# Kernel tuning notes

Hardware: AMD Instinct MI355X
Metric: run time of the kernel (lower is better)

The kernel has to match this reference:

```python
import jax, jax.numpy as jnp
import numpy as np

B, D, W, H = 512, 128, 256, 256  # batch, drive_num, window_size, hidden_size


def setup_inputs() -> dict:
    key = jax.random.key(0)
    k = jax.random.split(key, 7)
    x = jax.random.normal(k[0], (B, D, W), jnp.float32)
    # encode_attn: Linear(window_size + 2*hidden_size, 1)
    attn_w = jax.random.normal(k[1], (W + 2 * H,), jnp.float32) * 0.02
    attn_b = jax.random.normal(k[2], (), jnp.float32) * 0.02
    # single-layer LSTM, input_size=D, hidden_size=H; PyTorch gate order i,f,g,o
    W_ih = jax.random.normal(k[3], (4 * H, D), jnp.float32) * 0.05
    W_hh = jax.random.normal(k[4], (4 * H, H), jnp.float32) * 0.05
    b_ih = jax.random.normal(k[5], (4 * H,), jnp.float32) * 0.05
    b_hh = jax.random.normal(k[6], (4 * H,), jnp.float32) * 0.05
    return {"x": x, "attn_w": attn_w, "attn_b": attn_b,
            "W_ih": W_ih, "W_hh": W_hh, "b_ih": b_ih, "b_hh": b_hh}


def reference(x, attn_w, attn_b, W_ih, W_hh, b_ih, b_hh):
    # x: [B, D, W]
    h_dim = W_hh.shape[1]
    w_h = attn_w[:h_dim]           # weight on repeated hidden state
    w_c = attn_w[h_dim:2 * h_dim]  # weight on repeated cell state
    w_x = attn_w[2 * h_dim:]       # weight on full input row (constant over t)
    # precompute input contribution to attention logits: [B, D]
    e_x = jnp.einsum('bdw,w->bd', x, w_x) + attn_b
    x_steps = jnp.moveaxis(x, 2, 0)  # [W, B, D]

    def step(carry, x_t):
        h, c = carry  # [B, H] each
        # attention logit: h/c terms broadcast over drive dim
        e = e_x + (h @ w_h + c @ w_c)[:, None]  # [B, D]
        a = jax.nn.softmax(e, axis=-1)
        x_hat = a * x_t  # [B, D]
        gates = x_hat @ W_ih.T + b_ih + h @ W_hh.T + b_hh  # [B, 4H]
        i, f, g, o = jnp.split(gates, 4, axis=-1)
        c_new = jax.nn.sigmoid(f) * c + jax.nn.sigmoid(i) * jnp.tanh(g)
        h_new = jax.nn.sigmoid(o) * jnp.tanh(c_new)
        return (h_new, c_new), h_new

    bsz = x.shape[0]
    h0 = jnp.zeros((bsz, h_dim), x.dtype)
    c0 = jnp.zeros((bsz, h_dim), x.dtype)
    _, hs = jax.lax.scan(step, (h0, c0), x_steps)  # hs: [W, B, H]
    return jnp.transpose(hs, (1, 0, 2))  # [B, W, H] == hidden_states[:, 1:]
```

## Files before the change

### kernel.cpp

```cpp
#include <hip/hip_runtime.h>
#include <cstdint>

#define NB 512
#define ND 128
#define NW 256
#define NH 256
#define PGRP 32
#define QGRP 8

typedef _Float16 f16;
typedef _Float16 h8 __attribute__((ext_vector_type(8)));
typedef float f32x4 __attribute__((ext_vector_type(4)));

__device__ __forceinline__ float sigm(float v){ return 1.f/(1.f+__expf(-v)); }
__device__ __forceinline__ float tanh_fast(float v){
  v = fminf(fmaxf(v,-15.f),15.f);
  float e = __expf(2.f*v);
  return (e-1.f)/(e+1.f);
}

__global__ __launch_bounds__(128) void attn_kernel(
    const float* __restrict__ x, const float* __restrict__ attn_w,
    const float* __restrict__ attn_b, float* __restrict__ a_buf)
{
    __shared__ float wx[NW];
    __shared__ float sred[2];
    const int b = blockIdx.x;
    const int d = threadIdx.x;

    wx[d]       = attn_w[2 * NH + d];
    wx[d + 128] = attn_w[2 * NH + d + 128];
    __syncthreads();

    const float4* xr = (const float4*)(x + ((size_t)b * ND + d) * NW);
    float acc = 0.f;
    #pragma unroll 8
    for (int w4 = 0; w4 < NW / 4; ++w4) {
        float4 v = xr[w4];
        acc += v.x * wx[w4*4+0] + v.y * wx[w4*4+1]
             + v.z * wx[w4*4+2] + v.w * wx[w4*4+3];
    }
    float e = acc + attn_b[0];

    float mx = e;
    #pragma unroll
    for (int o = 32; o > 0; o >>= 1) mx = fmaxf(mx, __shfl_xor(mx, o));
    if ((d & 63) == 0) sred[d >> 6] = mx;
    __syncthreads();
    mx = fmaxf(sred[0], sred[1]);
    __syncthreads();

    float p = __expf(e - mx);
    float s = p;
    #pragma unroll
    for (int o = 32; o > 0; o >>= 1) s += __shfl_xor(s, o);
    if ((d & 63) == 0) sred[d >> 6] = s;
    __syncthreads();
    s = sred[0] + sred[1];

    a_buf[(size_t)b * ND + d] = p / s;
}

__global__ __launch_bounds__(512) void pack_kernel(
    const float* __restrict__ W_ih, const float* __restrict__ W_hh,
    const float* __restrict__ b_ih, const float* __restrict__ b_hh,
    f16* __restrict__ Wfrag, float* __restrict__ bias)
{
    int flat = blockIdx.x * 512 + threadIdx.x;
    int l    = flat & 63;
    int kt   = (flat >> 6) % 12;
    int wq   = (flat >> 6) / 12;
    int col16 = l & 15, kb = l >> 4;
    int hcol = (wq >> 3) * 32 + (wq & 7) * 4 + (col16 >> 2);
    int gate = col16 & 3;
    int n    = gate * 256 + hcol;
    int k0   = kt * 32 + kb * 8;

    f16 tmp[8];
    #pragma unroll
    for (int e = 0; e < 8; ++e) {
        int k = k0 + e;
        float v = (k < NH) ? W_hh[(size_t)n * NH + k]
                           : W_ih[(size_t)n * ND + (k - NH)];
        tmp[e] = (f16)v;
    }
    *(h8*)(Wfrag + (size_t)flat * 8) = *(const h8*)tmp;

    if (flat < 1024) bias[flat] = b_ih[flat] + b_hh[flat];
}

__global__ __launch_bounds__(512) void init_kernel(unsigned* __restrict__ flags)
{
    flags[blockIdx.x * 512 + threadIdx.x] = 0u;
}

__global__ __launch_bounds__(512, 2) void lstm_kernel(
    const float* __restrict__ x, const float* __restrict__ a_buf,
    const float* __restrict__ bias, const f16* __restrict__ Wfrag,
    f16* __restrict__ hx, unsigned* __restrict__ flags,
    float* __restrict__ out)
{
    __shared__ __align__(16) unsigned char A16[16 * 768];
    __shared__ float scr[8][272];

    const int tid = threadIdx.x;
    const int w = tid >> 6, l = tid & 63;
    const int p = blockIdx.x & 31, q = blockIdx.x >> 5;

    h8 bfrag[12];
    {
        const h8* wsrc = (const h8*)Wfrag + ((q * 8 + w) * 12) * 64 + l;
        #pragma unroll
        for (int kt = 0; kt < 12; ++kt) bfrag[kt] = wsrc[kt * 64];
    }

    const int m = l >> 2, hh = l & 3;
    const int jcol = q * 32 + w * 4 + hh;
    float bias4[4];
    #pragma unroll
    for (int g = 0; g < 4; ++g) bias4[g] = bias[g * 256 + jcol];
    float cstate = 0.f;

    float areg[8];
    const float* xbase = nullptr;
    const int xrow = tid >> 4, xdc = tid & 15;
    if (tid < 256) {
        int b = p * 16 + xrow;
        #pragma unroll
        for (int e = 0; e < 8; ++e) areg[e] = a_buf[b * ND + xdc * 8 + e];
        xbase = x + ((size_t)b * ND + xdc * 8) * NW;
    }
    const int r2 = tid >> 5, kc = tid & 31;
    const int arow = l & 15, akb = l >> 4;

    float4 xq[8];

    for (int t = 0; t < NW; ++t) {
        if (tid < 256 && (t & 3) == 0) {
            #pragma unroll
            for (int e = 0; e < 8; ++e)
                xq[e] = *(const float4*)(xbase + (size_t)e * NW + t);
        }
        if (tid < 256) {
            f16 xv[8];
            #pragma unroll
            for (int e = 0; e < 8; ++e) {
                float xf = xq[e].x;
                xq[e] = make_float4(xq[e].y, xq[e].z, xq[e].w, xq[e].x);
                xv[e] = (f16)(xf * areg[e]);
            }
            int byte = xrow * 768 + 512 + xdc * 16;
            byte ^= (xrow & 7) << 4;
            *(h8*)(A16 + byte) = *(const h8*)xv;
        }
        {
            int byte = r2 * 768 + kc * 16;
            byte ^= (r2 & 7) << 4;
            if (t == 0) {
                ((unsigned long long*)(A16 + byte))[0] = 0ull;
                ((unsigned long long*)(A16 + byte))[1] = 0ull;
            } else {
                while (__hip_atomic_load(&flags[(t - 1) * PGRP + p],
                                         __ATOMIC_RELAXED, __HIP_MEMORY_SCOPE_AGENT) < 8u) {}
                const unsigned long long* hrow = (const unsigned long long*)
                    (hx + ((size_t)((t - 1) & 1) * NB + p * 16 + r2) * NH);
                unsigned long long d0 = __hip_atomic_load(hrow + kc * 2 + 0,
                        __ATOMIC_RELAXED, __HIP_MEMORY_SCOPE_AGENT);
                unsigned long long d1 = __hip_atomic_load(hrow + kc * 2 + 1,
                        __ATOMIC_RELAXED, __HIP_MEMORY_SCOPE_AGENT);
                ((unsigned long long*)(A16 + byte))[0] = d0;
                ((unsigned long long*)(A16 + byte))[1] = d1;
            }
        }
        __syncthreads();

        f32x4 acc = {0.f, 0.f, 0.f, 0.f};
        #pragma unroll
        for (int kt = 0; kt < 12; ++kt) {
            int byte = arow * 768 + kt * 64 + akb * 16;
            byte ^= (arow & 7) << 4;
            h8 afrag = *(const h8*)(A16 + byte);
            acc = __builtin_amdgcn_mfma_f32_16x16x32_f16(afrag, bfrag[kt], acc, 0, 0, 0);
        }

        {
            float* sw = &scr[w][0];
            int col = l & 15, rb = (l >> 4) * 4;
            sw[(rb + 0) * 17 + col] = acc[0];
            sw[(rb + 1) * 17 + col] = acc[1];
            sw[(rb + 2) * 17 + col] = acc[2];
            sw[(rb + 3) * 17 + col] = acc[3];
            asm volatile("s_waitcnt lgkmcnt(0)" ::: "memory");
            float G0 = sw[m * 17 + hh * 4 + 0] + bias4[0];
            float G1 = sw[m * 17 + hh * 4 + 1] + bias4[1];
            float G2 = sw[m * 17 + hh * 4 + 2] + bias4[2];
            float G3 = sw[m * 17 + hh * 4 + 3] + bias4[3];
            float ig = sigm(G0), fg = sigm(G1);
            float gg = tanh_fast(G2), og = sigm(G3);
            cstate = fg * cstate + ig * gg;
            float hn = og * tanh_fast(cstate);

            int brow = p * 16 + m;
            __builtin_nontemporal_store(hn, &out[((size_t)brow * NW + t) * NH + jcol]);

            f16 hf = (f16)hn;
            unsigned short hb = __builtin_bit_cast(unsigned short, hf);
            int other = __shfl_xor((int)hb, 1);
            if (!(l & 1)) {
                unsigned val = (unsigned)hb | ((unsigned)(unsigned short)other << 16);
                unsigned* dst = (unsigned*)((unsigned short*)hx
                                + ((size_t)(t & 1) * NB + brow) * NH + jcol);
                __hip_atomic_store(dst, val, __ATOMIC_RELAXED, __HIP_MEMORY_SCOPE_AGENT);
            }
        }
        __syncthreads();
        if (tid == 0 && t < NW - 1)
            atomicAdd(&flags[t * PGRP + p], 1u);
    }
}

extern "C" void kernel_launch(void* const* d_in, const int* in_sizes, int n_in,
                              void* d_out, int out_size, void* d_ws, size_t ws_size,
                              hipStream_t stream) {
    (void)in_sizes; (void)n_in; (void)out_size;

    const float* x      = (const float*)d_in[0];
    const float* attn_w = (const float*)d_in[1];
    const float* attn_b = (const float*)d_in[2];
    const float* W_ih   = (const float*)d_in[3];
    const float* W_hh   = (const float*)d_in[4];
    const float* b_ih   = (const float*)d_in[5];
    const float* b_hh   = (const float*)d_in[6];
    float* out = (float*)d_out;

    char* ws = (char*)d_ws;
    float*    a_buf = (float*)ws;
    float*    bias  = (float*)(ws + 262144);
    f16*      Wfrag = (f16*)(ws + 266240);
    f16*      hx    = (f16*)(ws + 1052672);
    unsigned* flags = (unsigned*)(ws + 1576960);
    if (ws_size < (size_t)1609728) return;

    attn_kernel<<<NB, 128, 0, stream>>>(x, attn_w, attn_b, a_buf);
    pack_kernel<<<96, 512, 0, stream>>>(W_ih, W_hh, b_ih, b_hh, Wfrag, bias);
    init_kernel<<<16, 512, 0, stream>>>(flags);
    lstm_kernel<<<PGRP * QGRP, 512, 0, stream>>>(x, a_buf, bias, Wfrag, hx, flags, out);
}
```

Baseline: 828.3 us.

## Overlap x-part MFMAs with h wait and use per-block byte flags

Restructures the recurrent step so the input-projection MFMAs (k tiles 8..11) run before the next hidden state arrives, and the x staging for step t+1 is done after the flag publish instead of on the critical path. Replaces the atomicAdd counter with a u64 flag where each of the 8 column blocks sets its own byte, polled by a single thread against a full mask. The output store is also moved after the flag publish. This aims to shorten the per-step cross-block dependency latency, at the cost of an explicit vmcnt wait and a larger flag buffer, and it relies on byte stores into the u64 being seen correctly by the polling load.

```diff
diff --git a/kernel.cpp b/kernel.cpp
--- a/kernel.cpp
+++ b/kernel.cpp
@@ -11,6 +11,9 @@
 typedef _Float16 f16;
 typedef _Float16 h8 __attribute__((ext_vector_type(8)));
 typedef float f32x4 __attribute__((ext_vector_type(4)));
+typedef unsigned long long u64;
+
+#define FLAG_DONE 0x0101010101010101ull
 
 __device__ __forceinline__ float sigm(float v){ return 1.f/(1.f+__expf(-v)); }
 __device__ __forceinline__ float tanh_fast(float v){
@@ -97,7 +100,7 @@
 __global__ __launch_bounds__(512, 2) void lstm_kernel(
     const float* __restrict__ x, const float* __restrict__ a_buf,
     const float* __restrict__ bias, const f16* __restrict__ Wfrag,
-    f16* __restrict__ hx, unsigned* __restrict__ flags,
+    f16* __restrict__ hx, u64* __restrict__ flags,
     float* __restrict__ out)
 {
     __shared__ __align__(16) unsigned char A16[16 * 768];
@@ -135,54 +138,75 @@
 
     float4 xq[8];
 
+    {
+        int byte = r2 * 768 + kc * 16;
+        byte ^= (r2 & 7) << 4;
+        h8 z = {};
+        *(h8*)(A16 + byte) = z;
+    }
+    if (tid < 256) {
+        #pragma unroll
+        for (int e = 0; e < 8; ++e)
+            xq[e] = *(const float4*)(xbase + (size_t)e * NW);
+        f16 xv[8];
+        #pragma unroll
+        for (int e = 0; e < 8; ++e) {
+            float xf = xq[e].x;
+            xq[e] = make_float4(xq[e].y, xq[e].z, xq[e].w, xq[e].x);
+            xv[e] = (f16)(xf * areg[e]);
+        }
+        int byte = xrow * 768 + 512 + xdc * 16;
+        byte ^= (xrow & 7) << 4;
+        *(h8*)(A16 + byte) = *(const h8*)xv;
+    }
+
     for (int t = 0; t < NW; ++t) {
-        if (tid < 256 && (t & 3) == 0) {
+        if (t > 0 && tid == 0) {
+            while (__hip_atomic_load(&flags[(t - 1) * PGRP + p],
+                                     __ATOMIC_RELAXED, __HIP_MEMORY_SCOPE_AGENT)
+                   != FLAG_DONE) {}
+        }
+        __syncthreads();
+
+        f32x4 acc = {0.f, 0.f, 0.f, 0.f};
+        if (t > 0) {
+            const u64* hrow = (const u64*)
+                (hx + ((size_t)((t - 1) & 1) * NB + p * 16 + r2) * NH);
+            u64 d0 = __hip_atomic_load(hrow + kc * 2 + 0,
+                    __ATOMIC_RELAXED, __HIP_MEMORY_SCOPE_AGENT);
+            u64 d1 = __hip_atomic_load(hrow + kc * 2 + 1,
+                    __ATOMIC_RELAXED, __HIP_MEMORY_SCOPE_AGENT);
             #pragma unroll
-            for (int e = 0; e < 8; ++e)
-                xq[e] = *(const float4*)(xbase + (size_t)e * NW + t);
-        }
-        if (tid < 256) {
-            f16 xv[8];
-            #pragma unroll
-            for (int e = 0; e < 8; ++e) {
-                float xf = xq[e].x;
-                xq[e] = make_float4(xq[e].y, xq[e].z, xq[e].w, xq[e].x);
-                xv[e] = (f16)(xf * areg[e]);
-            }
-            int byte = xrow * 768 + 512 + xdc * 16;
-            byte ^= (xrow & 7) << 4;
-            *(h8*)(A16 + byte) = *(const h8*)xv;
-        }
-        {
+            for (int kt = 8; kt < 12; ++kt) {
+                int byte = arow * 768 + kt * 64 + akb * 16;
+                byte ^= (arow & 7) << 4;
+                h8 afrag = *(const h8*)(A16 + byte);
+                acc = __builtin_amdgcn_mfma_f32_16x16x32_f16(afrag, bfrag[kt], acc, 0, 0, 0);
+            }
             int byte = r2 * 768 + kc * 16;
             byte ^= (r2 & 7) << 4;
-            if (t == 0) {
-                ((unsigned long long*)(A16 + byte))[0] = 0ull;
-                ((unsigned long long*)(A16 + byte))[1] = 0ull;
-            } else {
-                while (__hip_atomic_load(&flags[(t - 1) * PGRP + p],
-                                         __ATOMIC_RELAXED, __HIP_MEMORY_SCOPE_AGENT) < 8u) {}
-                const unsigned long long* hrow = (const unsigned long long*)
-                    (hx + ((size_t)((t - 1) & 1) * NB + p * 16 + r2) * NH);
-                unsigned long long d0 = __hip_atomic_load(hrow + kc * 2 + 0,
-                        __ATOMIC_RELAXED, __HIP_MEMORY_SCOPE_AGENT);
-                unsigned long long d1 = __hip_atomic_load(hrow + kc * 2 + 1,
-                        __ATOMIC_RELAXED, __HIP_MEMORY_SCOPE_AGENT);
-                ((unsigned long long*)(A16 + byte))[0] = d0;
-                ((unsigned long long*)(A16 + byte))[1] = d1;
+            ((u64*)(A16 + byte))[0] = d0;
+            ((u64*)(A16 + byte))[1] = d1;
+        } else {
+            #pragma unroll
+            for (int kt = 8; kt < 12; ++kt) {
+                int byte = arow * 768 + kt * 64 + akb * 16;
+                byte ^= (arow & 7) << 4;
+                h8 afrag = *(const h8*)(A16 + byte);
+                acc = __builtin_amdgcn_mfma_f32_16x16x32_f16(afrag, bfrag[kt], acc, 0, 0, 0);
             }
         }
         __syncthreads();
 
-        f32x4 acc = {0.f, 0.f, 0.f, 0.f};
-        #pragma unroll
-        for (int kt = 0; kt < 12; ++kt) {
+        #pragma unroll
+        for (int kt = 0; kt < 8; ++kt) {
             int byte = arow * 768 + kt * 64 + akb * 16;
             byte ^= (arow & 7) << 4;
             h8 afrag = *(const h8*)(A16 + byte);
             acc = __builtin_amdgcn_mfma_f32_16x16x32_f16(afrag, bfrag[kt], acc, 0, 0, 0);
         }
 
+        float hn;
         {
             float* sw = &scr[w][0];
             int col = l & 15, rb = (l >> 4) * 4;
@@ -198,10 +222,7 @@
             float ig = sigm(G0), fg = sigm(G1);
             float gg = tanh_fast(G2), og = sigm(G3);
             cstate = fg * cstate + ig * gg;
-            float hn = og * tanh_fast(cstate);
-
-            int brow = p * 16 + m;
-            __builtin_nontemporal_store(hn, &out[((size_t)brow * NW + t) * NH + jcol]);
+            hn = og * tanh_fast(cstate);
 
             f16 hf = (f16)hn;
             unsigned short hb = __builtin_bit_cast(unsigned short, hf);
@@ -209,13 +230,38 @@
             if (!(l & 1)) {
                 unsigned val = (unsigned)hb | ((unsigned)(unsigned short)other << 16);
                 unsigned* dst = (unsigned*)((unsigned short*)hx
-                                + ((size_t)(t & 1) * NB + brow) * NH + jcol);
+                                + ((size_t)(t & 1) * NB + p * 16 + m) * NH + jcol);
                 __hip_atomic_store(dst, val, __ATOMIC_RELAXED, __HIP_MEMORY_SCOPE_AGENT);
             }
         }
+        asm volatile("s_waitcnt vmcnt(0)" ::: "memory");
         __syncthreads();
-        if (tid == 0 && t < NW - 1)
-            atomicAdd(&flags[t * PGRP + p], 1u);
+
+        if (tid == 0) {
+            unsigned char* fb = ((unsigned char*)&flags[t * PGRP + p]) + q;
+            __hip_atomic_store(fb, (unsigned char)1,
+                               __ATOMIC_RELAXED, __HIP_MEMORY_SCOPE_AGENT);
+        }
+
+        out[((size_t)(p * 16 + m) * NW + t) * NH + jcol] = hn;
+
+        if (tid < 256 && t + 1 < NW) {
+            if (((t + 1) & 3) == 0) {
+                #pragma unroll
+                for (int e = 0; e < 8; ++e)
+                    xq[e] = *(const float4*)(xbase + (size_t)e * NW + (t + 1));
+            }
+            f16 xv[8];
+            #pragma unroll
+            for (int e = 0; e < 8; ++e) {
+                float xf = xq[e].x;
+                xq[e] = make_float4(xq[e].y, xq[e].z, xq[e].w, xq[e].x);
+                xv[e] = (f16)(xf * areg[e]);
+            }
+            int byte = xrow * 768 + 512 + xdc * 16;
+            byte ^= (xrow & 7) << 4;
+            *(h8*)(A16 + byte) = *(const h8*)xv;
+        }
     }
 }
 
@@ -234,15 +280,15 @@
     float* out = (float*)d_out;
 
     char* ws = (char*)d_ws;
-    float*    a_buf = (float*)ws;
-    float*    bias  = (float*)(ws + 262144);
-    f16*      Wfrag = (f16*)(ws + 266240);
-    f16*      hx    = (f16*)(ws + 1052672);
-    unsigned* flags = (unsigned*)(ws + 1576960);
-    if (ws_size < (size_t)1609728) return;
+    float* a_buf = (float*)ws;
+    float* bias  = (float*)(ws + 262144);
+    f16*   Wfrag = (f16*)(ws + 266240);
+    f16*   hx    = (f16*)(ws + 1052672);
+    u64*   flags = (u64*)(ws + 1576960);
+    if (ws_size < (size_t)1642496) return;
 
     attn_kernel<<<NB, 128, 0, stream>>>(x, attn_w, attn_b, a_buf);
     pack_kernel<<<96, 512, 0, stream>>>(W_ih, W_hh, b_ih, b_hh, Wfrag, bias);
-    init_kernel<<<16, 512, 0, stream>>>(flags);
+    init_kernel<<<32, 512, 0, stream>>>((unsigned*)flags);
     lstm_kernel<<<PGRP * QGRP, 512, 0, stream>>>(x, a_buf, bias, Wfrag, hx, flags, out);
 }
```

Result: faster. 797.8 us (-3.7%).

## Replace flag counters with sentinel-poisoned hidden buffers and two-chunk interleaved blocks

Applied to the files above, without the earlier changes.

Drops the per-timestep flag counters. Consumers now spin directly on the fp16 hidden-state data until no word equals an Inf sentinel (0x7C00 pairs). Producers re-poison the slot three steps ahead in an 8-deep ring buffer. Each block now handles 32 batch rows as two interleaved 16-row phases with 4 waves over 16 hidden columns, so one chunk's latency can overlap the other's. The aim is to remove the flag round-trip and barrier serialization, at the cost of a vmcnt(0) drain per phase and relying on hidden values never exactly equalling the sentinel.

```diff
diff --git a/kernel.cpp b/kernel.cpp
--- a/kernel.cpp
+++ b/kernel.cpp
@@ -5,12 +5,13 @@
 #define ND 128
 #define NW 256
 #define NH 256
-#define PGRP 32
-#define QGRP 8
+#define SENT32 0x7C007C00u
+#define SENT64 0x7C007C007C007C00ull
 
 typedef _Float16 f16;
 typedef _Float16 h8 __attribute__((ext_vector_type(8)));
 typedef float f32x4 __attribute__((ext_vector_type(4)));
+typedef unsigned long long u64;
 
 __device__ __forceinline__ float sigm(float v){ return 1.f/(1.f+__expf(-v)); }
 __device__ __forceinline__ float tanh_fast(float v){
@@ -71,7 +72,7 @@
     int kt   = (flat >> 6) % 12;
     int wq   = (flat >> 6) / 12;
     int col16 = l & 15, kb = l >> 4;
-    int hcol = (wq >> 3) * 32 + (wq & 7) * 4 + (col16 >> 2);
+    int hcol = wq * 4 + (col16 >> 2);
     int gate = col16 & 3;
     int n    = gate * 256 + hcol;
     int k0   = kt * 32 + kb * 8;
@@ -89,134 +90,172 @@
     if (flat < 1024) bias[flat] = b_ih[flat] + b_hh[flat];
 }
 
-__global__ __launch_bounds__(512) void init_kernel(unsigned* __restrict__ flags)
-{
-    flags[blockIdx.x * 512 + threadIdx.x] = 0u;
-}
-
-__global__ __launch_bounds__(512, 2) void lstm_kernel(
+__global__ __launch_bounds__(512) void poison_kernel(uint4* __restrict__ hx4)
+{
+    uint4 v = {SENT32, SENT32, SENT32, SENT32};
+    hx4[(size_t)blockIdx.x * 512 + threadIdx.x] = v;
+}
+
+__global__ __launch_bounds__(256, 1) void lstm_kernel(
     const float* __restrict__ x, const float* __restrict__ a_buf,
     const float* __restrict__ bias, const f16* __restrict__ Wfrag,
-    f16* __restrict__ hx, unsigned* __restrict__ flags,
-    float* __restrict__ out)
-{
-    __shared__ __align__(16) unsigned char A16[16 * 768];
-    __shared__ float scr[8][272];
+    f16* __restrict__ hx, float* __restrict__ out)
+{
+    __shared__ __align__(16) unsigned char A16[2][16 * 768];
+    __shared__ float scr[4][272];
 
     const int tid = threadIdx.x;
     const int w = tid >> 6, l = tid & 63;
-    const int p = blockIdx.x & 31, q = blockIdx.x >> 5;
+    const int p2 = blockIdx.x & 15, q = blockIdx.x >> 4;
 
     h8 bfrag[12];
     {
-        const h8* wsrc = (const h8*)Wfrag + ((q * 8 + w) * 12) * 64 + l;
+        const h8* wsrc = (const h8*)Wfrag + ((q * 4 + w) * 12) * 64 + l;
         #pragma unroll
         for (int kt = 0; kt < 12; ++kt) bfrag[kt] = wsrc[kt * 64];
     }
 
     const int m = l >> 2, hh = l & 3;
-    const int jcol = q * 32 + w * 4 + hh;
+    const int jcol = q * 16 + w * 4 + hh;
     float bias4[4];
     #pragma unroll
     for (int g = 0; g < 4; ++g) bias4[g] = bias[g * 256 + jcol];
-    float cstate = 0.f;
-
-    float areg[8];
-    const float* xbase = nullptr;
+    float cst0 = 0.f, cst1 = 0.f;
+
     const int xrow = tid >> 4, xdc = tid & 15;
-    if (tid < 256) {
-        int b = p * 16 + xrow;
+    const int r2 = tid >> 4, kc = tid & 15;
+    const int arow = l & 15, akb = l >> 4;
+    const int pr = tid >> 2, pc = tid & 3;
+
+    float areg0[8], areg1[8];
+    const float* xbase0 = x + ((size_t)(p2 * 32 + xrow) * ND + xdc * 8) * NW;
+    const float* xbase1 = x + ((size_t)(p2 * 32 + 16 + xrow) * ND + xdc * 8) * NW;
+    #pragma unroll
+    for (int e = 0; e < 8; ++e) {
+        areg0[e] = a_buf[(p2 * 32 + xrow) * ND + xdc * 8 + e];
+        areg1[e] = a_buf[(p2 * 32 + 16 + xrow) * ND + xdc * 8 + e];
+    }
+    float4 xq0[8], xq1[8];
+
+    {
+        h8 z = {};
         #pragma unroll
-        for (int e = 0; e < 8; ++e) areg[e] = a_buf[b * ND + xdc * 8 + e];
-        xbase = x + ((size_t)b * ND + xdc * 8) * NW;
-    }
-    const int r2 = tid >> 5, kc = tid & 31;
-    const int arow = l & 15, akb = l >> 4;
-
-    float4 xq[8];
+        for (int c = 0; c < 2; ++c) {
+            int byte = c * 12288 + r2 * 768 + kc * 32;
+            *(h8*)(A16[0] + (byte ^ ((r2 & 7) << 4))) = z;
+            *(h8*)(A16[0] + ((byte + 16) ^ ((r2 & 7) << 4))) = z;
+        }
+    }
+    __syncthreads();
+
+    #define PHASE(C, CST, XQ, AREG, XBASE)                                        \
+    do {                                                                          \
+                                              \
+        if ((t & 3) == 0) {                                                       \
+            _Pragma("unroll")                                                     \
+            for (int e = 0; e < 8; ++e)                                           \
+                XQ[e] = *(const float4*)(XBASE + (size_t)e * NW + t);             \
+        }                                                                         \
+               \
+        {                                                                         \
+            f16 xv[8];                                                            \
+            _Pragma("unroll")                                                     \
+            for (int e = 0; e < 8; ++e) {                                         \
+                float xf = XQ[e].x;                                               \
+                XQ[e] = make_float4(XQ[e].y, XQ[e].z, XQ[e].w, XQ[e].x);          \
+                xv[e] = (f16)(xf * AREG[e]);                                      \
+            }                                                                     \
+            int byte = (C) * 12288 + xrow * 768 + 512 + xdc * 16;                 \
+            byte ^= (xrow & 7) << 4;                                              \
+            *(h8*)(A16[0] + byte) = *(const h8*)xv;                               \
+        }                                                                         \
+                       \
+        if (t > 0) {                                                              \
+            const u64* hrow = (const u64*)                                        \
+                (hx + ((size_t)((t - 1) & 7) * NB + p2 * 32 + (C) * 16 + r2) * NH); \
+            u64 d0, d1, d2, d3;                                                   \
+            for (;;) {                                                            \
+                d0 = __hip_atomic_load(hrow + kc * 4 + 0,                         \
+                        __ATOMIC_RELAXED, __HIP_MEMORY_SCOPE_AGENT);              \
+                d1 = __hip_atomic_load(hrow + kc * 4 + 1,                         \
+                        __ATOMIC_RELAXED, __HIP_MEMORY_SCOPE_AGENT);              \
+                d2 = __hip_atomic_load(hrow + kc * 4 + 2,                         \
+                        __ATOMIC_RELAXED, __HIP_MEMORY_SCOPE_AGENT);              \
+                d3 = __hip_atomic_load(hrow + kc * 4 + 3,                         \
+                        __ATOMIC_RELAXED, __HIP_MEMORY_SCOPE_AGENT);              \
+                if ((unsigned)d0 != SENT32 && (unsigned)(d0 >> 32) != SENT32 &&   \
+                    (unsigned)d1 != SENT32 && (unsigned)(d1 >> 32) != SENT32 &&   \
+                    (unsigned)d2 != SENT32 && (unsigned)(d2 >> 32) != SENT32 &&   \
+                    (unsigned)d3 != SENT32 && (unsigned)(d3 >> 32) != SENT32) break; \
+                __builtin_amdgcn_s_sleep(1);                                      \
+            }                                                                     \
+            int byte = (C) * 12288 + r2 * 768 + kc * 32;                          \
+            int b0 = byte ^ ((r2 & 7) << 4);                                      \
+            int b1 = (byte + 16) ^ ((r2 & 7) << 4);                               \
+            ((u64*)(A16[0] + b0))[0] = d0; ((u64*)(A16[0] + b0))[1] = d1;         \
+            ((u64*)(A16[0] + b1))[0] = d2; ((u64*)(A16[0] + b1))[1] = d3;         \
+        }                                                                         \
+        __syncthreads();                                        \
+                          \
+        f32x4 acc = {0.f, 0.f, 0.f, 0.f};                                         \
+        _Pragma("unroll")                                                         \
+        for (int kt = 0; kt < 12; ++kt) {                                         \
+            int byte = (C) * 12288 + arow * 768 + kt * 64 + akb * 16;             \
+            byte ^= (arow & 7) << 4;                                              \
+            h8 afrag = *(const h8*)(A16[0] + byte);                               \
+            acc = __builtin_amdgcn_mfma_f32_16x16x32_f16(afrag, bfrag[kt], acc, 0, 0, 0); \
+        }                                                                         \
+                        \
+        float hn;                                                                 \
+        {                                                                         \
+            float* sw = &scr[w][0];                                               \
+            int col = l & 15, rb = (l >> 4) * 4;                                  \
+            sw[(rb + 0) * 17 + col] = acc[0];                                     \
+            sw[(rb + 1) * 17 + col] = acc[1];                                     \
+            sw[(rb + 2) * 17 + col] = acc[2];                                     \
+            sw[(rb + 3) * 17 + col] = acc[3];                                     \
+            asm volatile("s_waitcnt lgkmcnt(0)" ::: "memory");                    \
+            float G0 = sw[m * 17 + hh * 4 + 0] + bias4[0];                        \
+            float G1 = sw[m * 17 + hh * 4 + 1] + bias4[1];                        \
+            float G2 = sw[m * 17 + hh * 4 + 2] + bias4[2];                        \
+            float G3 = sw[m * 17 + hh * 4 + 3] + bias4[3];                        \
+            float ig = sigm(G0), fg = sigm(G1);                                   \
+            float gg = tanh_fast(G2), og = sigm(G3);                              \
+            CST = fg * CST + ig * gg;                                             \
+            hn = og * tanh_fast(CST);                                             \
+        }                                                                         \
+                    \
+        {                                                                         \
+            f16 hf = (f16)hn;                                                     \
+            unsigned short hb = __builtin_bit_cast(unsigned short, hf);           \
+            int other = __shfl_xor((int)hb, 1);                                   \
+            if (!(l & 1)) {                                                       \
+                unsigned val = (unsigned)hb | ((unsigned)(unsigned short)other << 16); \
+                unsigned* dst = (unsigned*)((unsigned short*)hx                   \
+                    + ((size_t)(t & 7) * NB + p2 * 32 + (C) * 16 + m) * NH + jcol); \
+                __hip_atomic_store(dst, val,                                      \
+                        __ATOMIC_RELAXED, __HIP_MEMORY_SCOPE_AGENT);              \
+            }                                                                     \
+        }                                                                         \
+        out[((size_t)(p2 * 32 + (C) * 16 + m) * NW + t) * NH + jcol] = hn;        \
+               \
+        if (tid < 64) {                                                           \
+            u64* pb = (u64*)((unsigned short*)hx                                  \
+                + ((size_t)((t + 3) & 7) * NB + p2 * 32 + (C) * 16 + pr) * NH     \
+                + q * 16 + pc * 4);                                               \
+            __hip_atomic_store(pb, SENT64,                                        \
+                    __ATOMIC_RELAXED, __HIP_MEMORY_SCOPE_AGENT);                  \
+        }                                                                         \
+                \
+        asm volatile("s_waitcnt vmcnt(0)" ::: "memory");                          \
+        __syncthreads();                                                          \
+    } while (0)
 
     for (int t = 0; t < NW; ++t) {
-        if (tid < 256 && (t & 3) == 0) {
-            #pragma unroll
-            for (int e = 0; e < 8; ++e)
-                xq[e] = *(const float4*)(xbase + (size_t)e * NW + t);
-        }
-        if (tid < 256) {
-            f16 xv[8];
-            #pragma unroll
-            for (int e = 0; e < 8; ++e) {
-                float xf = xq[e].x;
-                xq[e] = make_float4(xq[e].y, xq[e].z, xq[e].w, xq[e].x);
-                xv[e] = (f16)(xf * areg[e]);
-            }
-            int byte = xrow * 768 + 512 + xdc * 16;
-            byte ^= (xrow & 7) << 4;
-            *(h8*)(A16 + byte) = *(const h8*)xv;
-        }
-        {
-            int byte = r2 * 768 + kc * 16;
-            byte ^= (r2 & 7) << 4;
-            if (t == 0) {
-                ((unsigned long long*)(A16 + byte))[0] = 0ull;
-                ((unsigned long long*)(A16 + byte))[1] = 0ull;
-            } else {
-                while (__hip_atomic_load(&flags[(t - 1) * PGRP + p],
-                                         __ATOMIC_RELAXED, __HIP_MEMORY_SCOPE_AGENT) < 8u) {}
-                const unsigned long long* hrow = (const unsigned long long*)
-                    (hx + ((size_t)((t - 1) & 1) * NB + p * 16 + r2) * NH);
-                unsigned long long d0 = __hip_atomic_load(hrow + kc * 2 + 0,
-                        __ATOMIC_RELAXED, __HIP_MEMORY_SCOPE_AGENT);
-                unsigned long long d1 = __hip_atomic_load(hrow + kc * 2 + 1,
-                        __ATOMIC_RELAXED, __HIP_MEMORY_SCOPE_AGENT);
-                ((unsigned long long*)(A16 + byte))[0] = d0;
-                ((unsigned long long*)(A16 + byte))[1] = d1;
-            }
-        }
-        __syncthreads();
-
-        f32x4 acc = {0.f, 0.f, 0.f, 0.f};
-        #pragma unroll
-        for (int kt = 0; kt < 12; ++kt) {
-            int byte = arow * 768 + kt * 64 + akb * 16;
-            byte ^= (arow & 7) << 4;
-            h8 afrag = *(const h8*)(A16 + byte);
-            acc = __builtin_amdgcn_mfma_f32_16x16x32_f16(afrag, bfrag[kt], acc, 0, 0, 0);
-        }
-
-        {
-            float* sw = &scr[w][0];
-            int col = l & 15, rb = (l >> 4) * 4;
-            sw[(rb + 0) * 17 + col] = acc[0];
-            sw[(rb + 1) * 17 + col] = acc[1];
-            sw[(rb + 2) * 17 + col] = acc[2];
-            sw[(rb + 3) * 17 + col] = acc[3];
-            asm volatile("s_waitcnt lgkmcnt(0)" ::: "memory");
-            float G0 = sw[m * 17 + hh * 4 + 0] + bias4[0];
-            float G1 = sw[m * 17 + hh * 4 + 1] + bias4[1];
-            float G2 = sw[m * 17 + hh * 4 + 2] + bias4[2];
-            float G3 = sw[m * 17 + hh * 4 + 3] + bias4[3];
-            float ig = sigm(G0), fg = sigm(G1);
-            float gg = tanh_fast(G2), og = sigm(G3);
-            cstate = fg * cstate + ig * gg;
-            float hn = og * tanh_fast(cstate);
-
-            int brow = p * 16 + m;
-            __builtin_nontemporal_store(hn, &out[((size_t)brow * NW + t) * NH + jcol]);
-
-            f16 hf = (f16)hn;
-            unsigned short hb = __builtin_bit_cast(unsigned short, hf);
-            int other = __shfl_xor((int)hb, 1);
-            if (!(l & 1)) {
-                unsigned val = (unsigned)hb | ((unsigned)(unsigned short)other << 16);
-                unsigned* dst = (unsigned*)((unsigned short*)hx
-                                + ((size_t)(t & 1) * NB + brow) * NH + jcol);
-                __hip_atomic_store(dst, val, __ATOMIC_RELAXED, __HIP_MEMORY_SCOPE_AGENT);
-            }
-        }
-        __syncthreads();
-        if (tid == 0 && t < NW - 1)
-            atomicAdd(&flags[t * PGRP + p], 1u);
-    }
+        PHASE(0, cst0, xq0, areg0, xbase0);
+        PHASE(1, cst1, xq1, areg1, xbase1);
+    }
+    #undef PHASE
 }
 
 extern "C" void kernel_launch(void* const* d_in, const int* in_sizes, int n_in,
@@ -234,15 +273,14 @@
     float* out = (float*)d_out;
 
     char* ws = (char*)d_ws;
-    float*    a_buf = (float*)ws;
-    float*    bias  = (float*)(ws + 262144);
-    f16*      Wfrag = (f16*)(ws + 266240);
-    f16*      hx    = (f16*)(ws + 1052672);
-    unsigned* flags = (unsigned*)(ws + 1576960);
-    if (ws_size < (size_t)1609728) return;
+    float* a_buf = (float*)ws;
+    float* bias  = (float*)(ws + 262144);
+    f16*   Wfrag = (f16*)(ws + 266240);
+    f16*   hx    = (f16*)(ws + 1052672);
+    if (ws_size < (size_t)3149824) return;
 
     attn_kernel<<<NB, 128, 0, stream>>>(x, attn_w, attn_b, a_buf);
     pack_kernel<<<96, 512, 0, stream>>>(W_ih, W_hh, b_ih, b_hh, Wfrag, bias);
-    init_kernel<<<16, 512, 0, stream>>>(flags);
-    lstm_kernel<<<PGRP * QGRP, 512, 0, stream>>>(x, a_buf, bias, Wfrag, hx, flags, out);
-}
+    poison_kernel<<<256, 512, 0, stream>>>((uint4*)hx);
+    lstm_kernel<<<256, 256, 0, stream>>>(x, a_buf, bias, Wfrag, hx, out);
+}
```

After: 1.087 ms. 31.2% more time.
